# Optimization experiments

Hardware: AMD Instinct MI355X
Metric: run time of the kernel (lower is better)

The kernel has to match this reference:

```python
import jax, jax.numpy as jnp
import numpy as np

N_NODES = 50000
N_EDGES = 800000
IN_CH = 128
OUT_CH = 32
HEADS = 4
NEG_SLOPE = 0.2


def setup_inputs() -> dict:
    key = jax.random.key(0)
    k = jax.random.split(key, 6)
    x = jax.random.normal(k[0], (N_NODES, IN_CH), dtype=jnp.float32)
    edge_index = jax.random.randint(k[1], (2, N_EDGES), 0, N_NODES, dtype=jnp.int32)
    # Glorot-style init for the learned parameters of GATConv
    W = jax.random.normal(k[2], (IN_CH, HEADS * OUT_CH), dtype=jnp.float32) / np.sqrt(IN_CH)
    att_src = jax.random.normal(k[3], (HEADS, OUT_CH), dtype=jnp.float32) / np.sqrt(OUT_CH)
    att_dst = jax.random.normal(k[4], (HEADS, OUT_CH), dtype=jnp.float32) / np.sqrt(OUT_CH)
    bias = jnp.zeros((HEADS * OUT_CH,), dtype=jnp.float32)
    return {"x": x, "edge_index": edge_index, "W": W,
            "att_src": att_src, "att_dst": att_dst, "bias": bias}


def reference(x, edge_index, W, att_src, att_dst, bias):
    # PyG GATConv, single layer: concat=True, add_self_loops=True, neg_slope=0.2
    N = x.shape[0]
    H, C = att_src.shape
    # add self loops (PyG default)
    loop = jnp.arange(N, dtype=edge_index.dtype)
    src = jnp.concatenate([edge_index[0], loop])  # [E+N] message sources j
    dst = jnp.concatenate([edge_index[1], loop])  # [E+N] message targets i
    # linear projection per head
    h = (x @ W).reshape(N, H, C)                  # [N,H,C]
    a_src = jnp.einsum('nhc,hc->nh', h, att_src)  # [N,H]
    a_dst = jnp.einsum('nhc,hc->nh', h, att_dst)  # [N,H]
    # edge-wise attention logits with LeakyReLU
    e = jax.nn.leaky_relu(a_src[src] + a_dst[dst], NEG_SLOPE)  # [E',H]
    # segment softmax over incoming edges of each destination node
    m = jax.ops.segment_max(e, dst, num_segments=N)            # [N,H]
    expe = jnp.exp(e - m[dst])
    denom = jax.ops.segment_sum(expe, dst, num_segments=N)     # [N,H]
    alpha = expe / denom[dst]                                  # [E',H]
    # scatter-aggregate weighted messages
    out = jax.ops.segment_sum(h[src] * alpha[:, :, None], dst, num_segments=N)  # [N,H,C]
    return out.reshape(N, H * C) + bias
```

## Files before the change

### kernel.cpp

```cpp
#include <hip/hip_runtime.h>


constexpr int N_NODES = 50000;
constexpr int N_EDGES = 800000;
constexpr int E_TOT   = N_EDGES + N_NODES;
constexpr int HC      = 128;
constexpr float NEG_SLOPE = 0.2f;
constexpr int M_TILES = N_NODES / 16;
constexpr int NB_GEMM = 512;
constexpr int NB_HIST = 512;
constexpr int SCAN_BLOCKS = (N_NODES + 1023) / 1024;

typedef short short8 __attribute__((ext_vector_type(8)));
typedef float f32x4  __attribute__((ext_vector_type(4)));

__device__ inline unsigned short f2bf(float f) {
    unsigned int u = __float_as_uint(f);
    u += 0x7FFF + ((u >> 16) & 1);
    return (unsigned short)(u >> 16);
}


__global__ __launch_bounds__(256) void gemm_hist(
    const float* __restrict__ x,
    const float* __restrict__ W,
    const float* __restrict__ att_src, const float* __restrict__ att_dst,
    const int* __restrict__ edst,
    unsigned short* __restrict__ hb,
    float* __restrict__ a_src, float* __restrict__ a_dst,
    int* __restrict__ deg, unsigned short* __restrict__ ppos)
{
    if (blockIdx.x >= NB_GEMM) {
        const int t0 = (blockIdx.x - NB_GEMM) * 256 + threadIdx.x;
        for (int e = t0; e < N_EDGES; e += NB_HIST * 256)
            ppos[e] = (unsigned short)atomicAdd(&deg[edst[e]], 1);
        return;
    }
    const int wave = threadIdx.x >> 6;
    const int lane = threadIdx.x & 63;
    const int n0   = (wave & 1) * 64;
    const int l15  = lane & 15;
    const int quad = lane >> 4;

    short8 bfrag[4][4];
    #pragma unroll
    for (int t = 0; t < 4; ++t)
        #pragma unroll
        for (int ks = 0; ks < 4; ++ks) {
            short8 b;
            #pragma unroll
            for (int j = 0; j < 8; ++j)
                b[j] = (short)f2bf(W[(ks * 32 + quad * 8 + j) * 128 + n0 + t * 16 + l15]);
            bfrag[t][ks] = b;
        }

    float asw[4], adw[4];
    #pragma unroll
    for (int t = 0; t < 4; ++t) {
        asw[t] = att_src[n0 + t * 16 + l15];
        adw[t] = att_dst[n0 + t * 16 + l15];
    }

    for (int mt = blockIdx.x * 2 + (wave >> 1); mt < M_TILES; mt += NB_GEMM * 2) {
        const int m0 = mt * 16;
        short8 afrag[4];
        #pragma unroll
        for (int ks = 0; ks < 4; ++ks) {
            const float4 u0 = *(const float4*)&x[(size_t)(m0 + l15) * 128 + ks * 32 + quad * 8];
            const float4 u1 = *(const float4*)&x[(size_t)(m0 + l15) * 128 + ks * 32 + quad * 8 + 4];
            short8 a;
            a[0] = (short)f2bf(u0.x); a[1] = (short)f2bf(u0.y);
            a[2] = (short)f2bf(u0.z); a[3] = (short)f2bf(u0.w);
            a[4] = (short)f2bf(u1.x); a[5] = (short)f2bf(u1.y);
            a[6] = (short)f2bf(u1.z); a[7] = (short)f2bf(u1.w);
            afrag[ks] = a;
        }

        f32x4 acc[4];
        #pragma unroll
        for (int t = 0; t < 4; ++t) acc[t] = (f32x4){0.f, 0.f, 0.f, 0.f};

        #pragma unroll
        for (int ks = 0; ks < 4; ++ks)
            #pragma unroll
            for (int t = 0; t < 4; ++t)
                acc[t] = __builtin_amdgcn_mfma_f32_16x16x32_bf16(afrag[ks], bfrag[t][ks], acc[t], 0, 0, 0);

        #pragma unroll
        for (int t = 0; t < 4; ++t)
            #pragma unroll
            for (int r = 0; r < 4; ++r)
                hb[(m0 + quad * 4 + r) * 128 + n0 + t * 16 + l15] = f2bf(acc[t][r]);

        float hs[2][4] = {{0.f,0.f,0.f,0.f},{0.f,0.f,0.f,0.f}};
        float hd[2][4] = {{0.f,0.f,0.f,0.f},{0.f,0.f,0.f,0.f}};
        #pragma unroll
        for (int t = 0; t < 4; ++t)
            #pragma unroll
            for (int r = 0; r < 4; ++r) {
                hs[t >> 1][r] += acc[t][r] * asw[t];
                hd[t >> 1][r] += acc[t][r] * adw[t];
            }
        #pragma unroll
        for (int off = 1; off < 16; off <<= 1)
            #pragma unroll
            for (int g = 0; g < 2; ++g)
                #pragma unroll
                for (int r = 0; r < 4; ++r) {
                    hs[g][r] += __shfl_xor(hs[g][r], off);
                    hd[g][r] += __shfl_xor(hd[g][r], off);
                }
        if (l15 == 0) {
            const int hb0 = n0 >> 5;
            #pragma unroll
            for (int g = 0; g < 2; ++g)
                #pragma unroll
                for (int r = 0; r < 4; ++r) {
                    a_src[(m0 + quad * 4 + r) * 4 + hb0 + g] = hs[g][r];
                    a_dst[(m0 + quad * 4 + r) * 4 + hb0 + g] = hd[g][r];
                }
        }
    }
}


__global__ __launch_bounds__(256) void scan(
    const int* __restrict__ deg, int* __restrict__ partial, int* __restrict__ bsum)
{
    __shared__ int wsum[4];
    const int tid  = threadIdx.x;
    const int lane = tid & 63;
    const int wv   = tid >> 6;
    const int base = blockIdx.x * 1024 + tid * 4;
    int d0 = 0, d1 = 0, d2 = 0, d3 = 0;
    if (base + 3 < N_NODES) {
        const int4 v = *(const int4*)&deg[base];
        d0 = v.x + 1; d1 = v.y + 1; d2 = v.z + 1; d3 = v.w + 1;
    } else {
        if (base + 0 < N_NODES) d0 = deg[base + 0] + 1;
        if (base + 1 < N_NODES) d1 = deg[base + 1] + 1;
        if (base + 2 < N_NODES) d2 = deg[base + 2] + 1;
        if (base + 3 < N_NODES) d3 = deg[base + 3] + 1;
    }
    const int s0 = d0, s1 = s0 + d1, s2 = s1 + d2, s3 = s2 + d3;
    int inc = s3;
    #pragma unroll
    for (int off = 1; off < 64; off <<= 1) {
        const int t = __shfl_up(inc, off);
        if (lane >= off) inc += t;
    }
    if (lane == 63) wsum[wv] = inc;
    __syncthreads();
    int wbase = 0;
    for (int k = 0; k < wv; ++k) wbase += wsum[k];
    const int tb = wbase + inc - s3;
    if (base + 3 < N_NODES) {
        *(int4*)&partial[base] = (int4){tb, tb + s0, tb + s1, tb + s2};
    } else {
        if (base + 0 < N_NODES) partial[base + 0] = tb;
        if (base + 1 < N_NODES) partial[base + 1] = tb + s0;
        if (base + 2 < N_NODES) partial[base + 2] = tb + s1;
        if (base + 3 < N_NODES) partial[base + 3] = tb + s2;
    }
    if (tid == 255) bsum[blockIdx.x] = wbase + inc;
}


__global__ __launch_bounds__(256) void scatter_fin(
    const int* __restrict__ esrc, const int* __restrict__ edst,
    const int* __restrict__ partial, const int* __restrict__ bsum,
    const unsigned short* __restrict__ ppos,
    int* __restrict__ row_st, unsigned short* __restrict__ csr_src)
{
    __shared__ int sb[64];
    if (threadIdx.x < 64) {
        const int v = (threadIdx.x < SCAN_BLOCKS) ? bsum[threadIdx.x] : 0;
        int s = v;
        #pragma unroll
        for (int off = 1; off < 64; off <<= 1) {
            const int t = __shfl_up(s, off);
            if ((int)threadIdx.x >= off) s += t;
        }
        sb[threadIdx.x] = s - v;
    }
    __syncthreads();
    const int idx = blockIdx.x * 256 + threadIdx.x;
    if (idx < N_EDGES) {
        const int d = edst[idx];
        csr_src[partial[d] + sb[d >> 10] + 1 + ppos[idx]] = (unsigned short)esrc[idx];
    } else if (idx < E_TOT) {
        const int i = idx - N_EDGES;
        const int r = partial[i] + sb[i >> 10];
        row_st[i] = r;
        csr_src[r] = (unsigned short)i;
        if (i == 0) row_st[N_NODES] = E_TOT;
    }
}


__global__ __launch_bounds__(256) void gat_agg(
    const int* __restrict__ row_start, const unsigned short* __restrict__ csr_src,
    const unsigned short* __restrict__ hb, const float* __restrict__ a_src,
    const float* __restrict__ a_dst, const float* __restrict__ bias,
    float* __restrict__ out)
{
    __shared__ float ws[4][256];
    const int wv = threadIdx.x >> 6;
    const int node = blockIdx.x * 4 + wv;
    if (node >= N_NODES) return;
    const int lane = threadIdx.x & 63;
    const int q    = lane >> 4;
    const int li   = lane & 15;
    const int ch0  = li * 8;
    const int hd   = li >> 2;
    const float4 ad4 = *(const float4*)&a_dst[node * 4];
    const int p0 = row_start[node], p1 = row_start[node + 1];

    float acc[8] = {0.f,0.f,0.f,0.f,0.f,0.f,0.f,0.f};
    float dsum = 0.f;

    for (int base = p0; base < p1; base += 64) {
        int m = p1 - base; if (m > 64) m = 64;
        int sv = 0;
        if (lane < m) {
            sv = (int)csr_src[base + lane];
            const float4 av = *(const float4*)&a_src[sv * 4];
            float t; float4 w4;
            t = av.x + ad4.x; t = t > 0.f ? t : NEG_SLOPE * t; w4.x = __expf(t);
            t = av.y + ad4.y; t = t > 0.f ? t : NEG_SLOPE * t; w4.y = __expf(t);
            t = av.z + ad4.z; t = t > 0.f ? t : NEG_SLOPE * t; w4.z = __expf(t);
            t = av.w + ad4.w; t = t > 0.f ? t : NEG_SLOPE * t; w4.w = __expf(t);
            *(float4*)&ws[wv][lane * 4] = w4;
        }
        const int i0 = (q < m) ? q : 0;
        int s_cur = __shfl(sv, i0);
        uint4 hv = *(const uint4*)&hb[(size_t)s_cur * 128 + ch0];
        for (int j = 0; j < m; j += 4) {
            const int ei  = j + q;
            const int idx = ei < m ? ei : j;
            const int ein = ei + 4;
            const int idxn = ein < m ? ein : 0;
            const int s_nxt = __shfl(sv, idxn);
            const uint4 hvn = *(const uint4*)&hb[(size_t)s_nxt * 128 + ch0];
            float w = ws[wv][idx * 4 + hd];
            if (ei >= m) w = 0.f;
            acc[0] += w * __uint_as_float(hv.x << 16);
            acc[1] += w * __uint_as_float(hv.x & 0xFFFF0000u);
            acc[2] += w * __uint_as_float(hv.y << 16);
            acc[3] += w * __uint_as_float(hv.y & 0xFFFF0000u);
            acc[4] += w * __uint_as_float(hv.z << 16);
            acc[5] += w * __uint_as_float(hv.z & 0xFFFF0000u);
            acc[6] += w * __uint_as_float(hv.w << 16);
            acc[7] += w * __uint_as_float(hv.w & 0xFFFF0000u);
            dsum += w;
            hv = hvn;
        }
    }
    #pragma unroll
    for (int off = 16; off <= 32; off <<= 1) {
        #pragma unroll
        for (int r = 0; r < 8; ++r) acc[r] += __shfl_xor(acc[r], off);
        dsum += __shfl_xor(dsum, off);
    }
    if (q == 0) {
        const float inv = 1.f / dsum;
        const float4 b0 = *(const float4*)&bias[ch0];
        const float4 b1 = *(const float4*)&bias[ch0 + 4];
        float4 o0, o1;
        o0.x = acc[0]*inv + b0.x; o0.y = acc[1]*inv + b0.y;
        o0.z = acc[2]*inv + b0.z; o0.w = acc[3]*inv + b0.w;
        o1.x = acc[4]*inv + b1.x; o1.y = acc[5]*inv + b1.y;
        o1.z = acc[6]*inv + b1.z; o1.w = acc[7]*inv + b1.w;
        *(float4*)&out[(size_t)node * HC + ch0]     = o0;
        *(float4*)&out[(size_t)node * HC + ch0 + 4] = o1;
    }
}

extern "C" void kernel_launch(void* const* d_in, const int* in_sizes, int n_in,
                              void* d_out, int out_size, void* d_ws, size_t ws_size,
                              hipStream_t stream) {
    const float* x       = (const float*)d_in[0];
    const int*   ei      = (const int*)  d_in[1];
    const float* W       = (const float*)d_in[2];
    const float* att_src = (const float*)d_in[3];
    const float* att_dst = (const float*)d_in[4];
    const float* bias    = (const float*)d_in[5];
    float* out = (float*)d_out;

    char* p = (char*)d_ws;
    unsigned short* hb  = (unsigned short*)p; p += (size_t)N_NODES * HC * 2;
    float* a_src = (float*)p; p += (size_t)N_NODES * 4 * 4;
    float* a_dst = (float*)p; p += (size_t)N_NODES * 4 * 4;
    unsigned short* csr_src = (unsigned short*)p; p += (size_t)E_TOT * 2;
    unsigned short* ppos    = (unsigned short*)p; p += (size_t)N_EDGES * 2;
    int* partial = (int*)p;   p += N_NODES * 4;
    int* row_st  = (int*)p;   p += (N_NODES + 4) * 4;
    int* deg     = (int*)p;   p += N_NODES * 4;
    int* bsum    = (int*)p;

    const int* esrc = ei;
    const int* edst = ei + N_EDGES;

    hipMemsetAsync(deg, 0, (size_t)N_NODES * sizeof(int), stream);

    gemm_hist  <<<NB_GEMM + NB_HIST, 256, 0, stream>>>(x, W, att_src, att_dst,
                                                       edst, hb, a_src, a_dst, deg, ppos);
    scan       <<<SCAN_BLOCKS, 256, 0, stream>>>(deg, partial, bsum);
    scatter_fin<<<(E_TOT + 255) / 256, 256, 0, stream>>>(esrc, edst, partial, bsum,
                                                         ppos, row_st, csr_src);
    gat_agg    <<<(N_NODES + 3) / 4, 256, 0, stream>>>(row_st, csr_src, hb, a_src,
                                                       a_dst, bias, out);
}
```

Baseline: 170.7 us.

## Fuse scan, CSR scatter and aggregation into one cooperative persistent kernel

Replaces the three separate scan, scatter and aggregation launches with a single cooperative kernel of 1024 persistent blocks that uses grid-wide syncs between phases. This targets per-launch overhead and the tail idle time between dependent kernels. It also rebalances the GEMM/histogram block split from 512/512 to 640/384. The costs are grid.sync overhead, an occupancy cap of 4 blocks per CU via launch bounds, and grid-stride loops in place of one block per work item.

```diff
diff --git a/kernel.cpp b/kernel.cpp
--- a/kernel.cpp
+++ b/kernel.cpp
@@ -1,4 +1,6 @@
 #include <hip/hip_runtime.h>
+#include <hip/hip_cooperative_groups.h>
+namespace cg = cooperative_groups;
 
 
 constexpr int N_NODES = 50000;
@@ -7,8 +9,9 @@
 constexpr int HC      = 128;
 constexpr float NEG_SLOPE = 0.2f;
 constexpr int M_TILES = N_NODES / 16;
-constexpr int NB_GEMM = 512;
-constexpr int NB_HIST = 512;
+constexpr int NB_GEMM = 640;
+constexpr int NB_HIST = 384;
+constexpr int NBLK    = 1024;
 constexpr int SCAN_BLOCKS = (N_NODES + 1023) / 1024;
 
 typedef short short8 __attribute__((ext_vector_type(8)));
@@ -124,155 +127,155 @@
 }
 
 
-__global__ __launch_bounds__(256) void scan(
-    const int* __restrict__ deg, int* __restrict__ partial, int* __restrict__ bsum)
-{
-    __shared__ int wsum[4];
-    const int tid  = threadIdx.x;
-    const int lane = tid & 63;
-    const int wv   = tid >> 6;
-    const int base = blockIdx.x * 1024 + tid * 4;
-    int d0 = 0, d1 = 0, d2 = 0, d3 = 0;
-    if (base + 3 < N_NODES) {
-        const int4 v = *(const int4*)&deg[base];
-        d0 = v.x + 1; d1 = v.y + 1; d2 = v.z + 1; d3 = v.w + 1;
-    } else {
-        if (base + 0 < N_NODES) d0 = deg[base + 0] + 1;
-        if (base + 1 < N_NODES) d1 = deg[base + 1] + 1;
-        if (base + 2 < N_NODES) d2 = deg[base + 2] + 1;
-        if (base + 3 < N_NODES) d3 = deg[base + 3] + 1;
-    }
-    const int s0 = d0, s1 = s0 + d1, s2 = s1 + d2, s3 = s2 + d3;
-    int inc = s3;
-    #pragma unroll
-    for (int off = 1; off < 64; off <<= 1) {
-        const int t = __shfl_up(inc, off);
-        if (lane >= off) inc += t;
-    }
-    if (lane == 63) wsum[wv] = inc;
-    __syncthreads();
-    int wbase = 0;
-    for (int k = 0; k < wv; ++k) wbase += wsum[k];
-    const int tb = wbase + inc - s3;
-    if (base + 3 < N_NODES) {
-        *(int4*)&partial[base] = (int4){tb, tb + s0, tb + s1, tb + s2};
-    } else {
-        if (base + 0 < N_NODES) partial[base + 0] = tb;
-        if (base + 1 < N_NODES) partial[base + 1] = tb + s0;
-        if (base + 2 < N_NODES) partial[base + 2] = tb + s1;
-        if (base + 3 < N_NODES) partial[base + 3] = tb + s2;
-    }
-    if (tid == 255) bsum[blockIdx.x] = wbase + inc;
-}
-
-
-__global__ __launch_bounds__(256) void scatter_fin(
+__global__ __launch_bounds__(256, 4) void gat_tail(
+    const int* __restrict__ deg,
     const int* __restrict__ esrc, const int* __restrict__ edst,
-    const int* __restrict__ partial, const int* __restrict__ bsum,
     const unsigned short* __restrict__ ppos,
-    int* __restrict__ row_st, unsigned short* __restrict__ csr_src)
-{
-    __shared__ int sb[64];
-    if (threadIdx.x < 64) {
-        const int v = (threadIdx.x < SCAN_BLOCKS) ? bsum[threadIdx.x] : 0;
-        int s = v;
-        #pragma unroll
-        for (int off = 1; off < 64; off <<= 1) {
-            const int t = __shfl_up(s, off);
-            if ((int)threadIdx.x >= off) s += t;
-        }
-        sb[threadIdx.x] = s - v;
-    }
-    __syncthreads();
-    const int idx = blockIdx.x * 256 + threadIdx.x;
-    if (idx < N_EDGES) {
-        const int d = edst[idx];
-        csr_src[partial[d] + sb[d >> 10] + 1 + ppos[idx]] = (unsigned short)esrc[idx];
-    } else if (idx < E_TOT) {
-        const int i = idx - N_EDGES;
-        const int r = partial[i] + sb[i >> 10];
-        row_st[i] = r;
-        csr_src[r] = (unsigned short)i;
-        if (i == 0) row_st[N_NODES] = E_TOT;
-    }
-}
-
-
-__global__ __launch_bounds__(256) void gat_agg(
-    const int* __restrict__ row_start, const unsigned short* __restrict__ csr_src,
+    int* __restrict__ partial, int* __restrict__ bsum,
+    int* __restrict__ row_st, unsigned short* __restrict__ csr_src,
     const unsigned short* __restrict__ hb, const float* __restrict__ a_src,
     const float* __restrict__ a_dst, const float* __restrict__ bias,
     float* __restrict__ out)
 {
-    __shared__ float ws[4][256];
-    const int wv = threadIdx.x >> 6;
-    const int node = blockIdx.x * 4 + wv;
-    if (node >= N_NODES) return;
-    const int lane = threadIdx.x & 63;
-    const int q    = lane >> 4;
-    const int li   = lane & 15;
-    const int ch0  = li * 8;
-    const int hd   = li >> 2;
-    const float4 ad4 = *(const float4*)&a_dst[node * 4];
-    const int p0 = row_start[node], p1 = row_start[node + 1];
-
-    float acc[8] = {0.f,0.f,0.f,0.f,0.f,0.f,0.f,0.f};
-    float dsum = 0.f;
-
-    for (int base = p0; base < p1; base += 64) {
-        int m = p1 - base; if (m > 64) m = 64;
-        int sv = 0;
-        if (lane < m) {
-            sv = (int)csr_src[base + lane];
-            const float4 av = *(const float4*)&a_src[sv * 4];
-            float t; float4 w4;
-            t = av.x + ad4.x; t = t > 0.f ? t : NEG_SLOPE * t; w4.x = __expf(t);
-            t = av.y + ad4.y; t = t > 0.f ? t : NEG_SLOPE * t; w4.y = __expf(t);
-            t = av.z + ad4.z; t = t > 0.f ? t : NEG_SLOPE * t; w4.z = __expf(t);
-            t = av.w + ad4.w; t = t > 0.f ? t : NEG_SLOPE * t; w4.w = __expf(t);
-            *(float4*)&ws[wv][lane * 4] = w4;
-        }
-        const int i0 = (q < m) ? q : 0;
-        int s_cur = __shfl(sv, i0);
-        uint4 hv = *(const uint4*)&hb[(size_t)s_cur * 128 + ch0];
-        for (int j = 0; j < m; j += 4) {
-            const int ei  = j + q;
-            const int idx = ei < m ? ei : j;
-            const int ein = ei + 4;
-            const int idxn = ein < m ? ein : 0;
-            const int s_nxt = __shfl(sv, idxn);
-            const uint4 hvn = *(const uint4*)&hb[(size_t)s_nxt * 128 + ch0];
-            float w = ws[wv][idx * 4 + hd];
-            if (ei >= m) w = 0.f;
-            acc[0] += w * __uint_as_float(hv.x << 16);
-            acc[1] += w * __uint_as_float(hv.x & 0xFFFF0000u);
-            acc[2] += w * __uint_as_float(hv.y << 16);
-            acc[3] += w * __uint_as_float(hv.y & 0xFFFF0000u);
-            acc[4] += w * __uint_as_float(hv.z << 16);
-            acc[5] += w * __uint_as_float(hv.z & 0xFFFF0000u);
-            acc[6] += w * __uint_as_float(hv.w << 16);
-            acc[7] += w * __uint_as_float(hv.w & 0xFFFF0000u);
-            dsum += w;
-            hv = hvn;
-        }
-    }
-    #pragma unroll
-    for (int off = 16; off <= 32; off <<= 1) {
-        #pragma unroll
-        for (int r = 0; r < 8; ++r) acc[r] += __shfl_xor(acc[r], off);
-        dsum += __shfl_xor(dsum, off);
-    }
-    if (q == 0) {
-        const float inv = 1.f / dsum;
-        const float4 b0 = *(const float4*)&bias[ch0];
-        const float4 b1 = *(const float4*)&bias[ch0 + 4];
-        float4 o0, o1;
-        o0.x = acc[0]*inv + b0.x; o0.y = acc[1]*inv + b0.y;
-        o0.z = acc[2]*inv + b0.z; o0.w = acc[3]*inv + b0.w;
-        o1.x = acc[4]*inv + b1.x; o1.y = acc[5]*inv + b1.y;
-        o1.z = acc[6]*inv + b1.z; o1.w = acc[7]*inv + b1.w;
-        *(float4*)&out[(size_t)node * HC + ch0]     = o0;
-        *(float4*)&out[(size_t)node * HC + ch0 + 4] = o1;
+    cg::grid_group grid = cg::this_grid();
+    const int blk  = blockIdx.x;
+    const int tid  = threadIdx.x;
+    const int wave = tid >> 6;
+    const int lane = tid & 63;
+    __shared__ int smi[1024];
+    float* smf = (float*)smi;
+
+    if (blk < SCAN_BLOCKS) {
+        const int base = blk * 1024 + tid * 4;
+        int d0 = 0, d1 = 0, d2 = 0, d3 = 0;
+        if (base + 3 < N_NODES) {
+            const int4 v = *(const int4*)&deg[base];
+            d0 = v.x + 1; d1 = v.y + 1; d2 = v.z + 1; d3 = v.w + 1;
+        } else {
+            if (base + 0 < N_NODES) d0 = deg[base + 0] + 1;
+            if (base + 1 < N_NODES) d1 = deg[base + 1] + 1;
+            if (base + 2 < N_NODES) d2 = deg[base + 2] + 1;
+            if (base + 3 < N_NODES) d3 = deg[base + 3] + 1;
+        }
+        const int s0 = d0, s1 = s0 + d1, s2 = s1 + d2, s3 = s2 + d3;
+        int inc = s3;
+        #pragma unroll
+        for (int off = 1; off < 64; off <<= 1) {
+            const int t = __shfl_up(inc, off);
+            if (lane >= off) inc += t;
+        }
+        if (lane == 63) smi[wave] = inc;
+        __syncthreads();
+        int wbase = 0;
+        for (int k = 0; k < wave; ++k) wbase += smi[k];
+        const int tb = wbase + inc - s3;
+        if (base + 3 < N_NODES) {
+            *(int4*)&partial[base] = (int4){tb, tb + s0, tb + s1, tb + s2};
+        } else {
+            if (base + 0 < N_NODES) partial[base + 0] = tb;
+            if (base + 1 < N_NODES) partial[base + 1] = tb + s0;
+            if (base + 2 < N_NODES) partial[base + 2] = tb + s1;
+            if (base + 3 < N_NODES) partial[base + 3] = tb + s2;
+        }
+        if (tid == 255) bsum[blk] = wbase + inc;
+    }
+    grid.sync();
+
+    {
+        if (tid < 64) {
+            const int v = (tid < SCAN_BLOCKS) ? bsum[tid] : 0;
+            int s = v;
+            #pragma unroll
+            for (int off = 1; off < 64; off <<= 1) {
+                const int t = __shfl_up(s, off);
+                if (tid >= off) s += t;
+            }
+            smi[tid] = s - v;
+        }
+        __syncthreads();
+        for (int idx = blk * 256 + tid; idx < E_TOT; idx += NBLK * 256) {
+            if (idx < N_EDGES) {
+                const int d = edst[idx];
+                csr_src[partial[d] + smi[d >> 10] + 1 + ppos[idx]] = (unsigned short)esrc[idx];
+            } else {
+                const int i = idx - N_EDGES;
+                const int r = partial[i] + smi[i >> 10];
+                row_st[i] = r;
+                csr_src[r] = (unsigned short)i;
+                if (i == 0) row_st[N_NODES] = E_TOT;
+            }
+        }
+    }
+    grid.sync();
+
+    float* ws = &smf[wave * 256];
+    const int q   = lane >> 4;
+    const int li  = lane & 15;
+    const int ch0 = li * 8;
+    const int hd  = li >> 2;
+    for (int nb = blk; nb < N_NODES / 4; nb += NBLK) {
+        const int node = nb * 4 + wave;
+        const float4 ad4 = *(const float4*)&a_dst[node * 4];
+        const int p0 = row_st[node], p1 = row_st[node + 1];
+
+        float acc[8] = {0.f,0.f,0.f,0.f,0.f,0.f,0.f,0.f};
+        float dsum = 0.f;
+
+        for (int base = p0; base < p1; base += 64) {
+            int m = p1 - base; if (m > 64) m = 64;
+            int sv = 0;
+            if (lane < m) {
+                sv = (int)csr_src[base + lane];
+                const float4 av = *(const float4*)&a_src[sv * 4];
+                float t; float4 w4;
+                t = av.x + ad4.x; t = t > 0.f ? t : NEG_SLOPE * t; w4.x = __expf(t);
+                t = av.y + ad4.y; t = t > 0.f ? t : NEG_SLOPE * t; w4.y = __expf(t);
+                t = av.z + ad4.z; t = t > 0.f ? t : NEG_SLOPE * t; w4.z = __expf(t);
+                t = av.w + ad4.w; t = t > 0.f ? t : NEG_SLOPE * t; w4.w = __expf(t);
+                *(float4*)&ws[lane * 4] = w4;
+            }
+            const int i0 = (q < m) ? q : 0;
+            int s_cur = __shfl(sv, i0);
+            uint4 hv = *(const uint4*)&hb[(size_t)s_cur * 128 + ch0];
+            for (int j = 0; j < m; j += 4) {
+                const int ei  = j + q;
+                const int idx = ei < m ? ei : j;
+                const int ein = ei + 4;
+                const int idxn = ein < m ? ein : 0;
+                const int s_nxt = __shfl(sv, idxn);
+                const uint4 hvn = *(const uint4*)&hb[(size_t)s_nxt * 128 + ch0];
+                float w = ws[idx * 4 + hd];
+                if (ei >= m) w = 0.f;
+                acc[0] += w * __uint_as_float(hv.x << 16);
+                acc[1] += w * __uint_as_float(hv.x & 0xFFFF0000u);
+                acc[2] += w * __uint_as_float(hv.y << 16);
+                acc[3] += w * __uint_as_float(hv.y & 0xFFFF0000u);
+                acc[4] += w * __uint_as_float(hv.z << 16);
+                acc[5] += w * __uint_as_float(hv.z & 0xFFFF0000u);
+                acc[6] += w * __uint_as_float(hv.w << 16);
+                acc[7] += w * __uint_as_float(hv.w & 0xFFFF0000u);
+                dsum += w;
+                hv = hvn;
+            }
+        }
+        #pragma unroll
+        for (int off = 16; off <= 32; off <<= 1) {
+            #pragma unroll
+            for (int r = 0; r < 8; ++r) acc[r] += __shfl_xor(acc[r], off);
+            dsum += __shfl_xor(dsum, off);
+        }
+        if (q == 0) {
+            const float inv = 1.f / dsum;
+            const float4 b0 = *(const float4*)&bias[ch0];
+            const float4 b1 = *(const float4*)&bias[ch0 + 4];
+            float4 o0, o1;
+            o0.x = acc[0]*inv + b0.x; o0.y = acc[1]*inv + b0.y;
+            o0.z = acc[2]*inv + b0.z; o0.w = acc[3]*inv + b0.w;
+            o1.x = acc[4]*inv + b1.x; o1.y = acc[5]*inv + b1.y;
+            o1.z = acc[6]*inv + b1.z; o1.w = acc[7]*inv + b1.w;
+            *(float4*)&out[(size_t)node * HC + ch0]     = o0;
+            *(float4*)&out[(size_t)node * HC + ch0 + 4] = o1;
+        }
     }
 }
 
@@ -296,18 +299,21 @@
     int* partial = (int*)p;   p += N_NODES * 4;
     int* row_st  = (int*)p;   p += (N_NODES + 4) * 4;
     int* deg     = (int*)p;   p += N_NODES * 4;
-    int* bsum    = (int*)p;
+    int* bsum    = (int*)p;   p += 64 * 4;
 
     const int* esrc = ei;
     const int* edst = ei + N_EDGES;
 
     hipMemsetAsync(deg, 0, (size_t)N_NODES * sizeof(int), stream);
 
-    gemm_hist  <<<NB_GEMM + NB_HIST, 256, 0, stream>>>(x, W, att_src, att_dst,
-                                                       edst, hb, a_src, a_dst, deg, ppos);
-    scan       <<<SCAN_BLOCKS, 256, 0, stream>>>(deg, partial, bsum);
-    scatter_fin<<<(E_TOT + 255) / 256, 256, 0, stream>>>(esrc, edst, partial, bsum,
-                                                         ppos, row_st, csr_src);
-    gat_agg    <<<(N_NODES + 3) / 4, 256, 0, stream>>>(row_st, csr_src, hb, a_src,
-                                                       a_dst, bias, out);
+    gemm_hist<<<NB_GEMM + NB_HIST, 256, 0, stream>>>(x, W, att_src, att_dst,
+                                                     edst, hb, a_src, a_dst, deg, ppos);
+
+    void* args[] = {
+        (void*)&deg, (void*)&esrc, (void*)&edst, (void*)&ppos,
+        (void*)&partial, (void*)&bsum, (void*)&row_st, (void*)&csr_src,
+        (void*)&hb, (void*)&a_src, (void*)&a_dst, (void*)&bias, (void*)&out
+    };
+    hipLaunchCooperativeKernel((const void*)gat_tail, dim3(NBLK), dim3(256),
+                               args, 0, stream);
 }
```

New measurement: 431.3 us. 153% more time.
